# Performance work log

Measured on AMD Instinct MI355X. Metric: run time of the kernel, lower is better.

The kernel has to match this reference:

```python
import jax, jax.numpy as jnp
import numpy as np

B, NX, NY = 4, 128, 128
DIM, DH, HEADS, LATENT, DOUT = 128, 64, 8, 64, 128
KM = 3
KD = DH * KM          # per-head low-rank-kernel dim (192)
SCALING = 1.0         # kernel_multiplier<=4 and softmax=False -> scaling_factor
ROT_SCALE = 64.0      # 1/min_freq of continuous RotaryEmbedding (min_freq=1/64)
EPS = 1e-5


def layer_norm(x, g, b):
    m = x.mean(-1, keepdims=True)
    v = jnp.var(x, axis=-1, keepdims=True)
    return (x - m) * jax.lax.rsqrt(v + EPS) * g + b


def pooling_reducer(x, Win, g, b, W1, b1, W2, b2):
    # x: [b, n, m, c] -> mean over axis 2 -> PreNorm(MLP with gated GELU) -> [b, n, latent]
    h = (x @ Win).mean(axis=2)
    h = layer_norm(h, g, b)
    h = h @ W1 + b1
    c = h.shape[-1] // 2
    h = jax.nn.gelu(h[..., :c], approximate=False) * h[..., c:]
    return h @ W2 + b2


def rotary(t, pos):
    # t: [b,h,n,d], pos: [n] continuous coordinates
    d = t.shape[-1]
    inv_freq = 1.0 / (10000.0 ** (jnp.arange(0, d, 2, dtype=jnp.float32) / d))
    f = (pos * ROT_SCALE)[:, None] * inv_freq          # [n, d//2]
    f = jnp.concatenate([f, f], axis=-1)               # [n, d]
    cos, sin = jnp.cos(f), jnp.sin(f)
    x1, x2 = jnp.split(t, 2, axis=-1)
    rot = jnp.concatenate([-x2, x1], axis=-1)          # rotate_half (half-split variant)
    return t * cos + rot * sin


def low_rank_kernel(u, pos, Wqk):
    # u: [b, n, latent] -> kernel K: [b, h, n, n]
    b, n, _ = u.shape
    qk = u @ Wqk                                       # [b, n, 2*h*KD]
    q, k = jnp.split(qk, 2, axis=-1)
    q = q.reshape(b, n, HEADS, KD).transpose(0, 2, 1, 3)
    k = k.reshape(b, n, HEADS, KD).transpose(0, 2, 1, 3)
    q = rotary(q, pos)
    k = rotary(k, pos)
    return jnp.einsum('bhid,bhjd->bhij', q, k) * SCALING


def setup_inputs():
    key = jax.random.key(0)
    ks = jax.random.split(key, 16)
    s = 0.02
    def rn(k, shape):
        return jax.random.normal(k, shape, dtype=jnp.float32) * s
    return {
        'u': jax.random.normal(ks[0], (B, NX, NY, DIM), dtype=jnp.float32),
        'pos_x': jnp.sort(jax.random.uniform(ks[1], (NX,), dtype=jnp.float32)),
        'pos_y': jnp.sort(jax.random.uniform(ks[2], (NY,), dtype=jnp.float32)),
        'ln_g': jnp.ones((DIM,), jnp.float32),
        'ln_b': jnp.zeros((DIM,), jnp.float32),
        'Wv': rn(ks[3], (DIM, HEADS * DH)),
        'Win': rn(ks[4], (DIM, DIM)),
        'px_Win': rn(ks[5], (DIM, DIM)),
        'px_g': jnp.ones((DIM,), jnp.float32),
        'px_b': jnp.zeros((DIM,), jnp.float32),
        'px_W1': rn(ks[6], (DIM, 2 * DIM)),
        'px_b1': jnp.zeros((2 * DIM,), jnp.float32),
        'px_W2': rn(ks[7], (DIM, LATENT)),
        'px_b2': jnp.zeros((LATENT,), jnp.float32),
        'py_Win': rn(ks[8], (DIM, DIM)),
        'py_g': jnp.ones((DIM,), jnp.float32),
        'py_b': jnp.zeros((DIM,), jnp.float32),
        'py_W1': rn(ks[9], (DIM, 2 * DIM)),
        'py_b1': jnp.zeros((2 * DIM,), jnp.float32),
        'py_W2': rn(ks[10], (DIM, LATENT)),
        'py_b2': jnp.zeros((LATENT,), jnp.float32),
        'Wqk_x': rn(ks[11], (LATENT, 2 * HEADS * KD)),
        'Wqk_y': rn(ks[12], (LATENT, 2 * HEADS * KD)),
        'Wo1': rn(ks[13], (HEADS * DH, DOUT)),
        'Wo2': rn(ks[14], (DOUT, DOUT)),
    }


def reference(u, pos_x, pos_y, ln_g, ln_b, Wv, Win,
              px_Win, px_g, px_b, px_W1, px_b1, px_W2, px_b2,
              py_Win, py_g, py_b, py_W1, py_b1, py_W2, py_b2,
              Wqk_x, Wqk_y, Wo1, Wo2):
    un = layer_norm(u, ln_g, ln_b)                      # [b,nx,ny,dim]
    v = un @ Wv                                         # [b,nx,ny,h*dh]
    ui = un @ Win
    ux = pooling_reducer(ui, px_Win, px_g, px_b, px_W1, px_b1, px_W2, px_b2)                       # [b,nx,L]
    uy = pooling_reducer(ui.transpose(0, 2, 1, 3), py_Win, py_g, py_b, py_W1, py_b1, py_W2, py_b2)  # [b,ny,L]
    kx = low_rank_kernel(ux, pos_x, Wqk_x)              # [b,h,nx,nx]
    ky = low_rank_kernel(uy, pos_y, Wqk_y)              # [b,h,ny,ny]
    b, nx, ny, _ = u.shape
    vphi = v.reshape(b, nx, ny, HEADS, DH).transpose(0, 3, 1, 2, 4)   # b h i l c
    t = jnp.einsum('bhij,bhjmc->bhimc', kx, vphi)       # attend along x axis
    t = jnp.einsum('bhlm,bhimc->bhilc', ky, t)          # attend along y axis
    t = t.transpose(0, 2, 3, 1, 4).reshape(b, nx, ny, HEADS * DH)
    # InstanceNorm2d applied to a channels-LAST tensor (as in the original repo):
    # torch treats dim1 (nx) as channels, normalizing over (ny, h*dh) per (b, nx), no affine.
    m = t.mean(axis=(2, 3), keepdims=True)
    var = t.var(axis=(2, 3), keepdims=True)
    t = (t - m) * jax.lax.rsqrt(var + EPS)
    h = jax.nn.gelu(t @ Wo1, approximate=False)
    return h @ Wo2
```

## Files before the change

kernel.cpp:

```cpp
#include <hip/hip_runtime.h>
#include <math.h>

#define KDD 192

typedef __attribute__((ext_vector_type(8))) short bfrag;
typedef __attribute__((ext_vector_type(4))) float facc;

__device__ inline unsigned short bf16r(float x) {
  union { float f; unsigned u; } v; v.f = x;
  unsigned r = v.u + 0x7fffu + ((v.u >> 16) & 1u);
  return (unsigned short)(r >> 16);
}
__device__ inline float bf2f(unsigned short h) {
  union { unsigned u; float f; } v; v.u = ((unsigned)h) << 16; return v.f;
}
__device__ inline float gelu_f(float x) {
  return x * 0.5f * (1.f + erff(x * 0.70710678f));
}
__device__ __forceinline__ void gload16(const void* g, void* l) {
  __builtin_amdgcn_global_load_lds((const __attribute__((address_space(1))) unsigned int*)g,
                                   (__attribute__((address_space(3))) unsigned int*)l,
                                   16, 0, 0);
}

__global__ __launch_bounds__(256) void k_lnw(const float* __restrict__ x,
                                             const float* __restrict__ g,
                                             const float* __restrict__ bb,
                                             unsigned short* __restrict__ y,
                                             const float* __restrict__ Wv,
                                             const float* __restrict__ Wo1,
                                             const float* __restrict__ Wo2,
                                             unsigned short* __restrict__ WvT,
                                             unsigned short* __restrict__ Wo1T,
                                             unsigned short* __restrict__ Wo2T,
                                             float* __restrict__ scol,
                                             const float* __restrict__ Win,
                                             const float* __restrict__ pxW,
                                             const float* __restrict__ pyW,
                                             float* __restrict__ Wcx,
                                             float* __restrict__ Wcy,
                                             const float* __restrict__ pos_x,
                                             const float* __restrict__ pos_y,
                                             float* __restrict__ tabx,
                                             float* __restrict__ taby) {
  __shared__ float As[16][64];
  __shared__ float Bs[16][64];
  int bid = blockIdx.x, t = threadIdx.x;
  if (bid < 16384) {
    int w = t >> 6, lane = t & 63;
    size_t row = (size_t)bid * 4 + w;
    float2 v = *(const float2*)(x + row * 128 + lane * 2);
    float s = v.x + v.y, s2 = v.x * v.x + v.y * v.y;
#pragma unroll
    for (int off = 1; off < 64; off <<= 1) {
      s += __shfl_xor(s, off, 64);
      s2 += __shfl_xor(s2, off, 64);
    }
    float mean = s * (1.f / 128.f);
    float var = s2 * (1.f / 128.f) - mean * mean;
    float r = rsqrtf(var + 1e-5f);
    float2 gg = *(const float2*)(g + lane * 2);
    float2 bv = *(const float2*)(bb + lane * 2);
    unsigned h0 = bf16r((v.x - mean) * r * gg.x + bv.x);
    unsigned h1 = bf16r((v.y - mean) * r * gg.y + bv.y);
    *(unsigned*)(y + row * 128 + lane * 2) = h0 | (h1 << 16);
    return;
  }
  if (bid < 16961) {
    int blk = bid - 16384;
    if (blk < 256) {
      int idx = blk * 256 + t;
      int c = idx >> 7, r = idx & 127;
      WvT[(size_t)c * 128 + r] = bf16r(Wv[(size_t)r * 512 + c]);
    } else if (blk < 512) {
      int idx = (blk - 256) * 256 + t;
      int n = idx >> 9, k = idx & 511;
      Wo1T[(size_t)n * 512 + k] = bf16r(Wo1[(size_t)k * 128 + n]);
    } else if (blk < 576) {
      int idx = (blk - 512) * 256 + t;
      int n = idx >> 7, k = idx & 127;
      Wo2T[n * 128 + k] = bf16r(Wo2[k * 128 + n]);
    } else {
      if (t < 128) {
        float a = 0;
        for (int k = 0; k < 512; k++) a += bf2f(bf16r(Wo1[k * 128 + t]));
        scol[t] = a;
      }
    }
    return;
  }
  if (bid < 16969) {
    int idx = bid - 16961;
    int n0 = (idx & 1) * 64, m0 = ((idx >> 1) & 1) * 64;
    const float* A = Win;
    const float* Bm = (idx >> 2) ? pyW : pxW;
    float* C = (idx >> 2) ? Wcy : Wcx;
    int tx = t & 15, ty = t >> 4;
    float acc[4][4] = {};
    int la_m = t >> 2, la_k = (t & 3) * 4;
    int lb_k = t >> 4, lb_n = (t & 15) * 4;
    for (int k0 = 0; k0 < 128; k0 += 16) {
      float4 a4 = *(const float4*)(A + (size_t)(m0 + la_m) * 128 + k0 + la_k);
      As[la_k + 0][la_m] = a4.x; As[la_k + 1][la_m] = a4.y;
      As[la_k + 2][la_m] = a4.z; As[la_k + 3][la_m] = a4.w;
      float4 b4 = *(const float4*)(Bm + (size_t)(k0 + lb_k) * 128 + n0 + lb_n);
      *(float4*)&Bs[lb_k][lb_n] = b4;
      __syncthreads();
#pragma unroll
      for (int kk = 0; kk < 16; kk++) {
        float4 av = *(const float4*)&As[kk][ty * 4];
        float4 bv = *(const float4*)&Bs[kk][tx * 4];
        float a[4] = {av.x, av.y, av.z, av.w};
        float b[4] = {bv.x, bv.y, bv.z, bv.w};
#pragma unroll
        for (int i = 0; i < 4; i++)
#pragma unroll
          for (int j = 0; j < 4; j++) acc[i][j] += a[i] * b[j];
      }
      __syncthreads();
    }
#pragma unroll
    for (int i = 0; i < 4; i++) {
      float4 o;
      o.x = acc[i][0]; o.y = acc[i][1]; o.z = acc[i][2]; o.w = acc[i][3];
      *(float4*)(C + (size_t)(m0 + ty * 4 + i) * 128 + n0 + tx * 4) = o;
    }
    return;
  }
  {
    int id = (bid - 16969) * 256 + t;
    int axis = id >= 12288;
    int rem = axis ? id - 12288 : id;
    int n = rem / 96, fi = rem - n * 96;
    const float* pos = axis ? pos_y : pos_x;
    float inv = expf(-logf(10000.f) * ((float)fi / 96.f));
    float f = pos[n] * 64.f * inv;
    float2 cssn;
    cssn.x = cosf(f);
    cssn.y = sinf(f);
    ((float2*)(axis ? taby : tabx))[n * 96 + fi] = cssn;
  }
}

__global__ __launch_bounds__(128) void k_pool2(const unsigned short* __restrict__ un,
                                               const float* __restrict__ Wc0, const float* __restrict__ Wc1,
                                               const float* __restrict__ g0, const float* __restrict__ g1,
                                               const float* __restrict__ bb0, const float* __restrict__ bb1,
                                               const float* __restrict__ W10, const float* __restrict__ W11,
                                               const float* __restrict__ b10, const float* __restrict__ b11,
                                               const float* __restrict__ W20, const float* __restrict__ W21,
                                               const float* __restrict__ b20, const float* __restrict__ b21,
                                               float* __restrict__ o0, float* __restrict__ o1) {
  int sel = blockIdx.y;
  const float* Wc = sel ? Wc1 : Wc0;
  const float* g = sel ? g1 : g0;     const float* bb = sel ? bb1 : bb0;
  const float* W1 = sel ? W11 : W10;  const float* b1 = sel ? b11 : b10;
  const float* W2 = sel ? W21 : W20;  const float* b2 = sel ? b21 : b20;
  float* out = sel ? o1 : o0;
  int row = blockIdx.x;
  int t = threadIdx.x;
  __shared__ float xin[128], h1[128], h3[128];
  __shared__ float ps[2], ps2[2];
  {
    float s0 = 0.f;
    if (sel == 0) {
      const unsigned short* p = un + (size_t)row * 16384 + t;
      for (int j = 0; j < 128; j++) s0 += bf2f(p[(size_t)j * 128]);
    } else {
      int b = row >> 7, j = row & 127;
      const unsigned short* p = un + (size_t)b * 2097152 + (size_t)j * 128 + t;
      for (int i = 0; i < 128; i++) s0 += bf2f(p[(size_t)i * 16384]);
    }
    xin[t] = s0 * (1.f / 128.f);
  }
  __syncthreads();
  float a = 0;
  for (int k = 0; k < 128; k++) a += xin[k] * Wc[k * 128 + t];
  float s = a, s2 = a * a;
  for (int off = 32; off > 0; off >>= 1) {
    s += __shfl_down(s, off, 64);
    s2 += __shfl_down(s2, off, 64);
  }
  if ((t & 63) == 0) { ps[t >> 6] = s; ps2[t >> 6] = s2; }
  __syncthreads();
  float S = ps[0] + ps[1], S2 = ps2[0] + ps2[1];
  float mean = S * (1.f / 128.f);
  float var = S2 * (1.f / 128.f) - mean * mean;
  float r = rsqrtf(var + 1e-5f);
  h1[t] = (a - mean) * r * g[t] + bb[t];
  __syncthreads();
  float u1 = b1[t], u2 = b1[t + 128];
  for (int k = 0; k < 128; k++) {
    float hv = h1[k];
    u1 += hv * W1[k * 256 + t];
    u2 += hv * W1[k * 256 + t + 128];
  }
  h3[t] = gelu_f(u1) * u2;
  __syncthreads();
  if (t < 64) {
    float o = b2[t];
    for (int k = 0; k < 128; k++) o += h3[k] * W2[k * 64 + t];
    out[(size_t)row * 64 + t] = o;
  }
}

__global__ __launch_bounds__(256) void k_gemmz(const float* __restrict__ A0,
                                               const float* __restrict__ B0,
                                               float* __restrict__ C0,
                                               const float* __restrict__ A1,
                                               const float* __restrict__ B1,
                                               float* __restrict__ C1,
                                               int K, int lda, int ldb, int ldc) {
  const float* A = blockIdx.z ? A1 : A0;
  const float* Bm = blockIdx.z ? B1 : B0;
  float* C = blockIdx.z ? C1 : C0;
  __shared__ float As[16][64];
  __shared__ float Bs[16][64];
  int tid = threadIdx.x;
  int n0 = blockIdx.x * 64, m0 = blockIdx.y * 64;
  int tx = tid & 15, ty = tid >> 4;
  float acc[4][4] = {};
  int la_m = tid >> 2, la_k = (tid & 3) * 4;
  int lb_k = tid >> 4, lb_n = (tid & 15) * 4;
  for (int k0 = 0; k0 < K; k0 += 16) {
    float4 a4 = *(const float4*)(A + (size_t)(m0 + la_m) * lda + k0 + la_k);
    As[la_k + 0][la_m] = a4.x; As[la_k + 1][la_m] = a4.y;
    As[la_k + 2][la_m] = a4.z; As[la_k + 3][la_m] = a4.w;
    float4 b4 = *(const float4*)(Bm + (size_t)(k0 + lb_k) * ldb + n0 + lb_n);
    *(float4*)&Bs[lb_k][lb_n] = b4;
    __syncthreads();
#pragma unroll
    for (int kk = 0; kk < 16; kk++) {
      float4 av = *(const float4*)&As[kk][ty * 4];
      float4 bv = *(const float4*)&Bs[kk][tx * 4];
      float a[4] = {av.x, av.y, av.z, av.w};
      float b[4] = {bv.x, bv.y, bv.z, bv.w};
#pragma unroll
      for (int i = 0; i < 4; i++)
#pragma unroll
        for (int j = 0; j < 4; j++) acc[i][j] += a[i] * b[j];
    }
    __syncthreads();
  }
#pragma unroll
  for (int i = 0; i < 4; i++) {
    float4 o;
    o.x = acc[i][0]; o.y = acc[i][1]; o.z = acc[i][2]; o.w = acc[i][3];
    *(float4*)(C + (size_t)(m0 + ty * 4 + i) * ldc + n0 + tx * 4) = o;
  }
}

__global__ __launch_bounds__(512) void k_qkt2(const float* __restrict__ qk0, const float* __restrict__ qk1,
                                              const float* __restrict__ tab0, const float* __restrict__ tab1,
                                              unsigned short* __restrict__ C0,
                                              unsigned short* __restrict__ C1) {
  int z = blockIdx.z;
  int bh = z & 31;
  int b = bh >> 3, h = bh & 7;
  const float* qk = (z < 32) ? qk0 : qk1;
  const float* tab = (z < 32) ? tab0 : tab1;
  unsigned short* Cb = ((z < 32) ? C0 : C1) + (size_t)bh * 16384;
  __shared__ float As[16][64];
  __shared__ float Bs[16][64];
  int tid = threadIdx.x;
  int i0 = blockIdx.y * 64, j0 = blockIdx.x * 64;
  int tx = tid & 15, ty = tid >> 4;
  float acc[2][4] = {};
  int l_m = tid >> 3, l_k = (tid & 7) * 2;
  for (int k0 = 0; k0 < KDD; k0 += 16) {
    int d = k0 + l_k;
    int fi = d < 96 ? d : d - 96;
    float sgn = d < 96 ? -1.f : 1.f;
    int prt = d < 96 ? d + 96 : d - 96;
    {
      int n = i0 + l_m;
      const float* src = qk + (size_t)(b * 128 + n) * 3072 + h * 192;
      float2 qd = *(const float2*)(src + d);
      float2 qp = *(const float2*)(src + prt);
      float2 t0 = *(const float2*)(tab + (size_t)(n * 96 + fi) * 2);
      float2 t1 = *(const float2*)(tab + (size_t)(n * 96 + fi + 1) * 2);
      As[l_k + 0][l_m] = qd.x * t0.x + sgn * qp.x * t0.y;
      As[l_k + 1][l_m] = qd.y * t1.x + sgn * qp.y * t1.y;
    }
    {
      int n = j0 + l_m;
      const float* src = qk + (size_t)(b * 128 + n) * 3072 + 1536 + h * 192;
      float2 qd = *(const float2*)(src + d);
      float2 qp = *(const float2*)(src + prt);
      float2 t0 = *(const float2*)(tab + (size_t)(n * 96 + fi) * 2);
      float2 t1 = *(const float2*)(tab + (size_t)(n * 96 + fi + 1) * 2);
      Bs[l_k + 0][l_m] = qd.x * t0.x + sgn * qp.x * t0.y;
      Bs[l_k + 1][l_m] = qd.y * t1.x + sgn * qp.y * t1.y;
    }
    __syncthreads();
#pragma unroll
    for (int kk = 0; kk < 16; kk++) {
      float2 av = *(const float2*)&As[kk][ty * 2];
      float4 bv = *(const float4*)&Bs[kk][tx * 4];
      float a[2] = {av.x, av.y};
      float b2[4] = {bv.x, bv.y, bv.z, bv.w};
#pragma unroll
      for (int i = 0; i < 2; i++)
#pragma unroll
        for (int j = 0; j < 4; j++) acc[i][j] += a[i] * b2[j];
    }
    __syncthreads();
  }
#pragma unroll
  for (int i = 0; i < 2; i++) {
    unsigned h0 = bf16r(acc[i][0]), h1 = bf16r(acc[i][1]);
    unsigned h2 = bf16r(acc[i][2]), h3 = bf16r(acc[i][3]);
    uint2 pk;
    pk.x = h0 | (h1 << 16);
    pk.y = h2 | (h3 << 16);
    *(uint2*)(Cb + (size_t)(i0 + ty * 2 + i) * 128 + j0 + tx * 4) = pk;
  }
}


__global__ __launch_bounds__(256) void k_vt(const unsigned short* __restrict__ WvT,
                                            const unsigned short* __restrict__ un,
                                            unsigned short* __restrict__ vT) {
  int nt = blockIdx.x;
  __shared__ __align__(16) unsigned short Bs[16384];
  int tid = threadIdx.x;
  int w = tid >> 6, lane = tid & 63, quad = lane >> 4, l16 = lane & 15;
  int wr = w >> 1, wc = w & 1;
  {
    const unsigned short* sbp = un + (size_t)nt * 16384;
#pragma unroll
    for (int q = 0; q < 8; q++) {
      int rbase = w * 32 + q * 4;
      int r = rbase + quad;
      gload16(sbp + (size_t)r * 128 + ((l16 ^ (r & 15)) << 3), &Bs[rbase * 128]);
    }
  }
  __syncthreads();
  facc zf = {0.f, 0.f, 0.f, 0.f};
#pragma unroll
  for (int mt = 0; mt < 4; mt++) {
    const unsigned short* ap = WvT + (size_t)mt * 128 * 128;
    facc acc[4][4];
#pragma unroll
    for (int lt = 0; lt < 4; lt++)
#pragma unroll
      for (int xt = 0; xt < 4; xt++) acc[lt][xt] = zf;
#pragma unroll
    for (int k0 = 0; k0 < 4; k0++) {
      int chunk = ((k0 * 4 + quad) ^ l16) << 3;
      bfrag bv[4], av[4];
#pragma unroll
      for (int lt = 0; lt < 4; lt++)
        bv[lt] = *(const bfrag*)&Bs[((wc * 4 + lt) * 16 + l16) * 128 + chunk];
#pragma unroll
      for (int xt = 0; xt < 4; xt++)
        av[xt] = *(const bfrag*)(ap + (size_t)((wr * 4 + xt) * 16 + l16) * 128 + k0 * 32 + quad * 8);
      __builtin_amdgcn_s_setprio(1);
#pragma unroll
      for (int lt = 0; lt < 4; lt++)
#pragma unroll
        for (int xt = 0; xt < 4; xt++)
          acc[lt][xt] = __builtin_amdgcn_mfma_f32_16x16x32_bf16(bv[lt], av[xt], acc[lt][xt], 0, 0, 0);
      __builtin_amdgcn_s_setprio(0);
    }
#pragma unroll
    for (int xt = 0; xt < 4; xt++) {
      int hc = mt * 128 + (wr * 4 + xt) * 16 + l16;
      unsigned short* dst = vT + (size_t)hc * 65536 + nt * 128 + quad * 4;
#pragma unroll
      for (int lt = 0; lt < 4; lt++) {
        facc a = acc[lt][xt];
        uint2 p;
        p.x = (unsigned)bf16r(a[0]) | ((unsigned)bf16r(a[1]) << 16);
        p.y = (unsigned)bf16r(a[2]) | ((unsigned)bf16r(a[3]) << 16);
        *(uint2*)(dst + (wc * 4 + lt) * 16) = p;
      }
    }
  }
}

__global__ __launch_bounds__(256, 2) void k_fuse12(const unsigned short* __restrict__ kxall,
                                                   const unsigned short* __restrict__ kyall,
                                                   const unsigned short* __restrict__ vT,
                                                   unsigned short* __restrict__ ttp,
                                                   float* __restrict__ sb,
                                                   float* __restrict__ s2b) {
  int blk = blockIdx.x;
  int bh = blk >> 4, strip = blk & 15;
  int b = bh >> 3, h = bh & 7;
  __shared__ __align__(16) unsigned short Ky[16384];
  __shared__ __align__(16) unsigned short Vs[16384];
  int tid = threadIdx.x;
  int w = tid >> 6, lane = tid & 63, quad = lane >> 4, l16 = lane & 15;
  int wr = w >> 1, wc = w & 1;

  {
    const unsigned short* kb = kyall + (size_t)bh * 16384;
#pragma unroll
    for (int q = 0; q < 8; q++) {
      int rbase = w * 32 + q * 4;
      int r = rbase + quad;
      gload16(kb + (size_t)r * 128 + ((l16 ^ (r & 15)) << 3), &Ky[rbase * 128]);
    }
  }
  bfrag axf[4][4];
  {
    const unsigned short* xb = kxall + (size_t)bh * 16384;
#pragma unroll
    for (int it = 0; it < 4; it++) {
      int i = (wr * 4 + it) * 16 + l16;
#pragma unroll
      for (int k0 = 0; k0 < 4; k0++)
        axf[it][k0] = *(const bfrag*)(xb + (size_t)i * 128 + k0 * 32 + quad * 8);
    }
  }

  float s[4] = {0.f, 0.f, 0.f, 0.f}, s2[4] = {0.f, 0.f, 0.f, 0.f};
  facc zf = {0.f, 0.f, 0.f, 0.f};

  for (int cc = 0; cc < 4; cc++) {
    int c = strip * 4 + cc;
    if (cc) __syncthreads();
    {
      const unsigned short* vb = vT + (size_t)(h * 64 + c) * 65536 + (size_t)b * 16384;
#pragma unroll
      for (int q = 0; q < 8; q++) {
        int rbase = w * 32 + q * 4;
        int r = rbase + quad;
        gload16(vb + (size_t)r * 128 + ((l16 ^ (r & 15)) << 3), &Vs[rbase * 128]);
      }
    }
    __syncthreads();

    facc a1[4][4];
#pragma unroll
    for (int xt = 0; xt < 4; xt++)
#pragma unroll
      for (int lt = 0; lt < 4; lt++) a1[xt][lt] = zf;
#pragma unroll
    for (int k0 = 0; k0 < 4; k0++) {
      int chunk = ((k0 * 4 + quad) ^ l16) << 3;
      bfrag av[4], bv[4];
#pragma unroll
      for (int xt = 0; xt < 4; xt++)
        av[xt] = *(const bfrag*)&Vs[((wr * 4 + xt) * 16 + l16) * 128 + chunk];
#pragma unroll
      for (int lt = 0; lt < 4; lt++)
        bv[lt] = *(const bfrag*)&Ky[((wc * 4 + lt) * 16 + l16) * 128 + chunk];
      __builtin_amdgcn_s_setprio(1);
#pragma unroll
      for (int xt = 0; xt < 4; xt++)
#pragma unroll
        for (int lt = 0; lt < 4; lt++)
          a1[xt][lt] = __builtin_amdgcn_mfma_f32_16x16x32_bf16(av[xt], bv[lt], a1[xt][lt], 0, 0, 0);
      __builtin_amdgcn_s_setprio(0);
    }
    __syncthreads();
#pragma unroll
    for (int xt = 0; xt < 4; xt++) {
      int xc = (wr * 4 + xt) * 2 + (quad >> 1);
      int xo = (quad & 1) * 4;
#pragma unroll
      for (int lt = 0; lt < 4; lt++) {
        int l = (wc * 4 + lt) * 16 + l16;
        unsigned p0 = (unsigned)bf16r(a1[xt][lt][0]) | ((unsigned)bf16r(a1[xt][lt][1]) << 16);
        unsigned p1 = (unsigned)bf16r(a1[xt][lt][2]) | ((unsigned)bf16r(a1[xt][lt][3]) << 16);
        uint2 p; p.x = p0; p.y = p1;
        *(uint2*)&Vs[l * 128 + ((xc ^ (l & 15)) << 3) + xo] = p;
      }
    }
    __syncthreads();

    facc a2[4][4];
#pragma unroll
    for (int st = 0; st < 4; st++)
#pragma unroll
      for (int it = 0; it < 4; it++) a2[st][it] = zf;
#pragma unroll
    for (int k0 = 0; k0 < 4; k0++) {
      int chunk = ((k0 * 4 + quad) ^ l16) << 3;
      bfrag sv[4];
#pragma unroll
      for (int st = 0; st < 4; st++)
        sv[st] = *(const bfrag*)&Vs[((wc * 4 + st) * 16 + l16) * 128 + chunk];
      __builtin_amdgcn_s_setprio(1);
#pragma unroll
      for (int st = 0; st < 4; st++)
#pragma unroll
        for (int it = 0; it < 4; it++)
          a2[st][it] = __builtin_amdgcn_mfma_f32_16x16x32_bf16(sv[st], axf[it][k0], a2[st][it], 0, 0, 0);
      __builtin_amdgcn_s_setprio(0);
    }
    {
      unsigned short* dst = ttp + ((size_t)(bh * 64 + c) << 14);
#pragma unroll
      for (int st = 0; st < 4; st++) {
        int l0 = (wc * 4 + st) * 16 + quad * 4;
#pragma unroll
        for (int it = 0; it < 4; it++) {
          int i = (wr * 4 + it) * 16 + l16;
          float f0 = a2[st][it][0], f1 = a2[st][it][1];
          float f2 = a2[st][it][2], f3 = a2[st][it][3];
          unsigned p0 = (unsigned)bf16r(f0) | ((unsigned)bf16r(f1) << 16);
          unsigned p1 = (unsigned)bf16r(f2) | ((unsigned)bf16r(f3) << 16);
          uint2 p; p.x = p0; p.y = p1;
          *(uint2*)(dst + (size_t)i * 128 + l0) = p;
          s[it] += (f0 + f1) + (f2 + f3);
          s2[it] += f0 * f0 + f1 * f1 + f2 * f2 + f3 * f3;
        }
      }
    }
  }
#pragma unroll
  for (int it = 0; it < 4; it++) {
    float v = s[it], v2 = s2[it];
    v += __shfl_xor(v, 16, 64);  v += __shfl_xor(v, 32, 64);
    v2 += __shfl_xor(v2, 16, 64); v2 += __shfl_xor(v2, 32, 64);
    if (quad == 0) {
      int i = (wr * 4 + it) * 16 + l16;
      atomicAdd(&sb[b * 128 + i], v);
      atomicAdd(&s2b[b * 128 + i], v2);
    }
  }
}

__global__ __launch_bounds__(256) void k_tail2(const unsigned short* __restrict__ ttp,
                                               const unsigned short* __restrict__ Wo1T,
                                               const unsigned short* __restrict__ Wo2T,
                                               float* __restrict__ out,
                                               const float* __restrict__ sb,
                                               const float* __restrict__ s2b,
                                               const float* __restrict__ sc) {
  int blk = blockIdx.x;
  int b = blk >> 7, i = blk & 127;
  __shared__ __align__(16) unsigned short As[16384];
  __shared__ __align__(16) unsigned short Bs[16384];
  int tid = threadIdx.x;
  int w = tid >> 6, lane = tid & 63, quad = lane >> 4, l16 = lane & 15;
  facc zf = {0.f, 0.f, 0.f, 0.f};
  facc a1[2][8];
#pragma unroll
  for (int a = 0; a < 2; a++)
#pragma unroll
    for (int bq = 0; bq < 8; bq++) a1[a][bq] = zf;
  for (int kc = 0; kc < 4; kc++) {
    if (kc) __syncthreads();
    {
      int r = tid >> 1, half = tid & 1;
      int hc = kc * 128 + r;
      const unsigned short* src = ttp + (((size_t)(b * 8 + (hc >> 6)) * 64 + (hc & 63)) * 128 + i) * 128 + half * 64;
#pragma unroll
      for (int q = 0; q < 8; q++) {
        uint4 v = *(const uint4*)(src + q * 8);
        unsigned short* pv = (unsigned short*)&v;
#pragma unroll
        for (int e = 0; e < 8; e++) {
          int l = half * 64 + q * 8 + e;
          As[l * 128 + (((r >> 3) ^ (l & 15)) << 3) + (r & 7)] = pv[e];
        }
      }
      const unsigned short* sB = Wo1T + (size_t)r * 512 + kc * 128 + half * 64;
#pragma unroll
      for (int q = 0; q < 8; q++) {
        int c8 = half * 8 + q;
        *(uint4*)&Bs[r * 128 + ((c8 ^ (r & 15)) << 3)] = *(const uint4*)(sB + q * 8);
      }
    }
    __syncthreads();
#pragma unroll
    for (int k0 = 0; k0 < 4; k0++) {
      bfrag av[2];
#pragma unroll
      for (int it = 0; it < 2; it++) {
        int row = (w + it * 4) * 16 + l16;
        av[it] = *(const bfrag*)&As[row * 128 + (((k0 * 4 + quad) ^ l16) << 3)];
      }
#pragma unroll
      for (int nt = 0; nt < 8; nt++) {
        int row = nt * 16 + l16;
        bfrag bv = *(const bfrag*)&Bs[row * 128 + (((k0 * 4 + quad) ^ l16) << 3)];
        a1[0][nt] = __builtin_amdgcn_mfma_f32_16x16x32_bf16(av[0], bv, a1[0][nt], 0, 0, 0);
        a1[1][nt] = __builtin_amdgcn_mfma_f32_16x16x32_bf16(av[1], bv, a1[1][nt], 0, 0, 0);
      }
    }
  }
  float S = sb[b * 128 + i], S2 = s2b[b * 128 + i];
  float mean = S * (1.f / 65536.f);
  float var = S2 * (1.f / 65536.f) - mean * mean;
  float rs = rsqrtf(var + 1e-5f);
  __syncthreads();
#pragma unroll
  for (int it = 0; it < 2; it++)
#pragma unroll
    for (int nt = 0; nt < 8; nt++) {
      int n1 = nt * 16 + l16;
      float scn = sc[n1];
#pragma unroll
      for (int rr = 0; rr < 4; rr++) {
        int l = (w + it * 4) * 16 + quad * 4 + rr;
        float val = (a1[it][nt][rr] - mean * scn) * rs;
        As[l * 128 + (((n1 >> 3) ^ (l & 15)) << 3) + (n1 & 7)] = bf16r(gelu_f(val));
      }
    }
  {
    int r = tid >> 1, half = tid & 1;
    const unsigned short* sB = Wo2T + (size_t)r * 128 + half * 64;
#pragma unroll
    for (int q = 0; q < 8; q++) {
      int c8 = half * 8 + q;
      *(uint4*)&Bs[r * 128 + ((c8 ^ (r & 15)) << 3)] = *(const uint4*)(sB + q * 8);
    }
  }
  __syncthreads();
  facc a2[2][8];
#pragma unroll
  for (int a = 0; a < 2; a++)
#pragma unroll
    for (int bq = 0; bq < 8; bq++) a2[a][bq] = zf;
#pragma unroll
  for (int k0 = 0; k0 < 4; k0++) {
    bfrag av[2];
#pragma unroll
    for (int it = 0; it < 2; it++) {
      int row = (w + it * 4) * 16 + l16;
      av[it] = *(const bfrag*)&As[row * 128 + (((k0 * 4 + quad) ^ l16) << 3)];
    }
#pragma unroll
    for (int nt = 0; nt < 8; nt++) {
      int row = nt * 16 + l16;
      bfrag bv = *(const bfrag*)&Bs[row * 128 + (((k0 * 4 + quad) ^ l16) << 3)];
      a2[0][nt] = __builtin_amdgcn_mfma_f32_16x16x32_bf16(av[0], bv, a2[0][nt], 0, 0, 0);
      a2[1][nt] = __builtin_amdgcn_mfma_f32_16x16x32_bf16(av[1], bv, a2[1][nt], 0, 0, 0);
    }
  }
#pragma unroll
  for (int it = 0; it < 2; it++)
#pragma unroll
    for (int nt = 0; nt < 8; nt++) {
      int n2 = nt * 16 + l16;
#pragma unroll
      for (int rr = 0; rr < 4; rr++) {
        int l = (w + it * 4) * 16 + quad * 4 + rr;
        out[((size_t)(b * 16384 + i * 128 + l)) * 128 + n2] = a2[it][nt][rr];
      }
    }
}

extern "C" void kernel_launch(void* const* d_in, const int* in_sizes, int n_in,
                              void* d_out, int out_size, void* d_ws, size_t ws_size,
                              hipStream_t stream) {
  const float* u = (const float*)d_in[0];
  const float* pos_x = (const float*)d_in[1];
  const float* pos_y = (const float*)d_in[2];
  const float* ln_g = (const float*)d_in[3];
  const float* ln_b = (const float*)d_in[4];
  const float* Wv = (const float*)d_in[5];
  const float* Win = (const float*)d_in[6];
  const float* px_Win = (const float*)d_in[7];
  const float* px_g = (const float*)d_in[8];
  const float* px_b = (const float*)d_in[9];
  const float* px_W1 = (const float*)d_in[10];
  const float* px_b1 = (const float*)d_in[11];
  const float* px_W2 = (const float*)d_in[12];
  const float* px_b2 = (const float*)d_in[13];
  const float* py_Win = (const float*)d_in[14];
  const float* py_g = (const float*)d_in[15];
  const float* py_b = (const float*)d_in[16];
  const float* py_W1 = (const float*)d_in[17];
  const float* py_b1 = (const float*)d_in[18];
  const float* py_W2 = (const float*)d_in[19];
  const float* py_b2 = (const float*)d_in[20];
  const float* Wqk_x = (const float*)d_in[21];
  const float* Wqk_y = (const float*)d_in[22];
  const float* Wo1 = (const float*)d_in[23];
  const float* Wo2 = (const float*)d_in[24];
  float* out = (float*)d_out;

  const size_t NEED = 44868736;
  if (ws_size < NEED * sizeof(float)) return;
  float* ws = (float*)d_ws;
  unsigned short* un_bf = (unsigned short*)ws;
  unsigned short* vT    = (unsigned short*)(ws + 4194304);
  unsigned short* ttp   = (unsigned short*)(ws + 20971520);
  float* small = ws + 37748736;
  float* Wcx   = small + 131072;
  float* Wcy   = small + 147456;
  float* ux    = small + 163840;
  float* uy    = small + 196608;
  float* qkx   = small + 229376;
  float* qky   = small + 1802240;
  float* tabx  = small + 3375104;
  float* taby  = small + 3399680;
  unsigned short* kx_bf = (unsigned short*)(small + 6520832);
  unsigned short* ky_bf = (unsigned short*)(small + 6782976);
  unsigned short* WvT   = (unsigned short*)(small + 7045120);
  unsigned short* Wo1T  = (unsigned short*)(small + 7077888);
  unsigned short* Wo2T  = (unsigned short*)(small + 7110656);
  float* sbuf  = small + 7118848;
  float* s2buf = small + 7119360;
  float* scol  = small + 7119872;

  hipMemsetAsync(sbuf, 0, 1024 * sizeof(float), stream);

  k_lnw<<<17065, 256, 0, stream>>>(u, ln_g, ln_b, un_bf, Wv, Wo1, Wo2,
                                   WvT, Wo1T, Wo2T, scol,
                                   Win, px_Win, py_Win, Wcx, Wcy,
                                   pos_x, pos_y, tabx, taby);
  k_pool2<<<dim3(512, 2), 128, 0, stream>>>(un_bf, Wcx, Wcy, px_g, py_g, px_b, py_b,
                                            px_W1, py_W1, px_b1, py_b1, px_W2, py_W2,
                                            px_b2, py_b2, ux, uy);
  k_gemmz<<<dim3(48, 8, 2), 256, 0, stream>>>(ux, Wqk_x, qkx, uy, Wqk_y, qky,
                                              64, 64, 3072, 3072);
  k_qkt2<<<dim3(2, 2, 64), 512, 0, stream>>>(qkx, qky, tabx, taby, kx_bf, ky_bf);

  k_vt<<<512, 256, 0, stream>>>(WvT, un_bf, vT);
  k_fuse12<<<512, 256, 0, stream>>>(kx_bf, ky_bf, vT, ttp, sbuf, s2buf);
  k_tail2<<<512, 256, 0, stream>>>(ttp, Wo1T, Wo2T, out, sbuf, s2buf, scol);
}
```

Before: 296.3 us.

## Merge pooling into V-projection kernel, fold memset into LN, pack tail transpose stores

Drops the separate memset by having an extra block of the LN kernel zero the statistics buffer. The pooling-reducer kernel and the V-projection GEMM now share one launch, with each pooling block handling two rows, which removes a kernel and lets the two independent stages run at once. The tail kernel's transposed LDS staging now writes two rows per 32-bit store instead of single 16-bit stores. The cost is a larger shared-memory footprint for the pooling blocks, which carry the GEMM's LDS allocation.

```diff
diff --git a/kernel.cpp b/kernel.cpp
--- a/kernel.cpp
+++ b/kernel.cpp
@@ -42,7 +42,8 @@
                                              const float* __restrict__ pos_x,
                                              const float* __restrict__ pos_y,
                                              float* __restrict__ tabx,
-                                             float* __restrict__ taby) {
+                                             float* __restrict__ taby,
+                                             float* __restrict__ sbuf) {
   __shared__ float As[16][64];
   __shared__ float Bs[16][64];
   int bid = blockIdx.x, t = threadIdx.x;
@@ -127,7 +128,7 @@
     }
     return;
   }
-  {
+  if (bid < 17065) {
     int id = (bid - 16969) * 256 + t;
     int axis = id >= 12288;
     int rem = axis ? id - 12288 : id;
@@ -139,28 +140,96 @@
     cssn.x = cosf(f);
     cssn.y = sinf(f);
     ((float2*)(axis ? taby : tabx))[n * 96 + fi] = cssn;
-  }
-}
-
-__global__ __launch_bounds__(128) void k_pool2(const unsigned short* __restrict__ un,
-                                               const float* __restrict__ Wc0, const float* __restrict__ Wc1,
-                                               const float* __restrict__ g0, const float* __restrict__ g1,
-                                               const float* __restrict__ bb0, const float* __restrict__ bb1,
-                                               const float* __restrict__ W10, const float* __restrict__ W11,
-                                               const float* __restrict__ b10, const float* __restrict__ b11,
-                                               const float* __restrict__ W20, const float* __restrict__ W21,
-                                               const float* __restrict__ b20, const float* __restrict__ b21,
-                                               float* __restrict__ o0, float* __restrict__ o1) {
-  int sel = blockIdx.y;
+    return;
+  }
+  {
+    float4 z4 = {0.f, 0.f, 0.f, 0.f};
+    ((float4*)sbuf)[t] = z4;
+  }
+}
+
+__global__ __launch_bounds__(256) void k_pvt(const unsigned short* __restrict__ WvT,
+                                             const unsigned short* __restrict__ un,
+                                             unsigned short* __restrict__ vT,
+                                             const float* __restrict__ Wc0, const float* __restrict__ Wc1,
+                                             const float* __restrict__ g0, const float* __restrict__ g1,
+                                             const float* __restrict__ bb0, const float* __restrict__ bb1,
+                                             const float* __restrict__ W10, const float* __restrict__ W11,
+                                             const float* __restrict__ b10, const float* __restrict__ b11,
+                                             const float* __restrict__ W20, const float* __restrict__ W21,
+                                             const float* __restrict__ b20, const float* __restrict__ b21,
+                                             float* __restrict__ o0, float* __restrict__ o1) {
+  __shared__ __align__(16) unsigned short Bs[16384];
+  __shared__ float xin[2][128], h1[2][128], h3[2][128];
+  __shared__ float ps[2][2], ps2[2][2];
+  int bid = blockIdx.x;
+  int tid = threadIdx.x;
+  if (bid < 512) {
+    int nt = bid;
+    int w = tid >> 6, lane = tid & 63, quad = lane >> 4, l16 = lane & 15;
+    int wr = w >> 1, wc = w & 1;
+    {
+      const unsigned short* sbp = un + (size_t)nt * 16384;
+#pragma unroll
+      for (int q = 0; q < 8; q++) {
+        int rbase = w * 32 + q * 4;
+        int r = rbase + quad;
+        gload16(sbp + (size_t)r * 128 + ((l16 ^ (r & 15)) << 3), &Bs[rbase * 128]);
+      }
+    }
+    __syncthreads();
+    facc zf = {0.f, 0.f, 0.f, 0.f};
+#pragma unroll
+    for (int mt = 0; mt < 4; mt++) {
+      const unsigned short* ap = WvT + (size_t)mt * 128 * 128;
+      facc acc[4][4];
+#pragma unroll
+      for (int lt = 0; lt < 4; lt++)
+#pragma unroll
+        for (int xt = 0; xt < 4; xt++) acc[lt][xt] = zf;
+#pragma unroll
+      for (int k0 = 0; k0 < 4; k0++) {
+        int chunk = ((k0 * 4 + quad) ^ l16) << 3;
+        bfrag bv[4], av[4];
+#pragma unroll
+        for (int lt = 0; lt < 4; lt++)
+          bv[lt] = *(const bfrag*)&Bs[((wc * 4 + lt) * 16 + l16) * 128 + chunk];
+#pragma unroll
+        for (int xt = 0; xt < 4; xt++)
+          av[xt] = *(const bfrag*)(ap + (size_t)((wr * 4 + xt) * 16 + l16) * 128 + k0 * 32 + quad * 8);
+        __builtin_amdgcn_s_setprio(1);
+#pragma unroll
+        for (int lt = 0; lt < 4; lt++)
+#pragma unroll
+          for (int xt = 0; xt < 4; xt++)
+            acc[lt][xt] = __builtin_amdgcn_mfma_f32_16x16x32_bf16(bv[lt], av[xt], acc[lt][xt], 0, 0, 0);
+        __builtin_amdgcn_s_setprio(0);
+      }
+#pragma unroll
+      for (int xt = 0; xt < 4; xt++) {
+        int hc = mt * 128 + (wr * 4 + xt) * 16 + l16;
+        unsigned short* dst = vT + (size_t)hc * 65536 + nt * 128 + quad * 4;
+#pragma unroll
+        for (int lt = 0; lt < 4; lt++) {
+          facc a = acc[lt][xt];
+          uint2 p;
+          p.x = (unsigned)bf16r(a[0]) | ((unsigned)bf16r(a[1]) << 16);
+          p.y = (unsigned)bf16r(a[2]) | ((unsigned)bf16r(a[3]) << 16);
+          *(uint2*)(dst + (wc * 4 + lt) * 16) = p;
+        }
+      }
+    }
+    return;
+  }
+  int u2 = tid >> 7;
+  int t = tid & 127;
+  int unit = (bid - 512) * 2 + u2;
+  int sel = unit >> 9, row = unit & 511;
   const float* Wc = sel ? Wc1 : Wc0;
   const float* g = sel ? g1 : g0;     const float* bb = sel ? bb1 : bb0;
   const float* W1 = sel ? W11 : W10;  const float* b1 = sel ? b11 : b10;
   const float* W2 = sel ? W21 : W20;  const float* b2 = sel ? b21 : b20;
   float* out = sel ? o1 : o0;
-  int row = blockIdx.x;
-  int t = threadIdx.x;
-  __shared__ float xin[128], h1[128], h3[128];
-  __shared__ float ps[2], ps2[2];
   {
     float s0 = 0.f;
     if (sel == 0) {
@@ -171,35 +240,35 @@
       const unsigned short* p = un + (size_t)b * 2097152 + (size_t)j * 128 + t;
       for (int i = 0; i < 128; i++) s0 += bf2f(p[(size_t)i * 16384]);
     }
-    xin[t] = s0 * (1.f / 128.f);
+    xin[u2][t] = s0 * (1.f / 128.f);
   }
   __syncthreads();
   float a = 0;
-  for (int k = 0; k < 128; k++) a += xin[k] * Wc[k * 128 + t];
+  for (int k = 0; k < 128; k++) a += xin[u2][k] * Wc[k * 128 + t];
   float s = a, s2 = a * a;
   for (int off = 32; off > 0; off >>= 1) {
     s += __shfl_down(s, off, 64);
     s2 += __shfl_down(s2, off, 64);
   }
-  if ((t & 63) == 0) { ps[t >> 6] = s; ps2[t >> 6] = s2; }
+  if ((t & 63) == 0) { ps[u2][t >> 6] = s; ps2[u2][t >> 6] = s2; }
   __syncthreads();
-  float S = ps[0] + ps[1], S2 = ps2[0] + ps2[1];
+  float S = ps[u2][0] + ps[u2][1], S2 = ps2[u2][0] + ps2[u2][1];
   float mean = S * (1.f / 128.f);
   float var = S2 * (1.f / 128.f) - mean * mean;
   float r = rsqrtf(var + 1e-5f);
-  h1[t] = (a - mean) * r * g[t] + bb[t];
+  h1[u2][t] = (a - mean) * r * g[t] + bb[t];
   __syncthreads();
-  float u1 = b1[t], u2 = b1[t + 128];
+  float u1 = b1[t], uu2 = b1[t + 128];
   for (int k = 0; k < 128; k++) {
-    float hv = h1[k];
+    float hv = h1[u2][k];
     u1 += hv * W1[k * 256 + t];
-    u2 += hv * W1[k * 256 + t + 128];
-  }
-  h3[t] = gelu_f(u1) * u2;
+    uu2 += hv * W1[k * 256 + t + 128];
+  }
+  h3[u2][t] = gelu_f(u1) * uu2;
   __syncthreads();
   if (t < 64) {
     float o = b2[t];
-    for (int k = 0; k < 128; k++) o += h3[k] * W2[k * 64 + t];
+    for (int k = 0; k < 128; k++) o += h3[u2][k] * W2[k * 64 + t];
     out[(size_t)row * 64 + t] = o;
   }
 }
@@ -318,67 +387,6 @@
 }
 
 
-__global__ __launch_bounds__(256) void k_vt(const unsigned short* __restrict__ WvT,
-                                            const unsigned short* __restrict__ un,
-                                            unsigned short* __restrict__ vT) {
-  int nt = blockIdx.x;
-  __shared__ __align__(16) unsigned short Bs[16384];
-  int tid = threadIdx.x;
-  int w = tid >> 6, lane = tid & 63, quad = lane >> 4, l16 = lane & 15;
-  int wr = w >> 1, wc = w & 1;
-  {
-    const unsigned short* sbp = un + (size_t)nt * 16384;
-#pragma unroll
-    for (int q = 0; q < 8; q++) {
-      int rbase = w * 32 + q * 4;
-      int r = rbase + quad;
-      gload16(sbp + (size_t)r * 128 + ((l16 ^ (r & 15)) << 3), &Bs[rbase * 128]);
-    }
-  }
-  __syncthreads();
-  facc zf = {0.f, 0.f, 0.f, 0.f};
-#pragma unroll
-  for (int mt = 0; mt < 4; mt++) {
-    const unsigned short* ap = WvT + (size_t)mt * 128 * 128;
-    facc acc[4][4];
-#pragma unroll
-    for (int lt = 0; lt < 4; lt++)
-#pragma unroll
-      for (int xt = 0; xt < 4; xt++) acc[lt][xt] = zf;
-#pragma unroll
-    for (int k0 = 0; k0 < 4; k0++) {
-      int chunk = ((k0 * 4 + quad) ^ l16) << 3;
-      bfrag bv[4], av[4];
-#pragma unroll
-      for (int lt = 0; lt < 4; lt++)
-        bv[lt] = *(const bfrag*)&Bs[((wc * 4 + lt) * 16 + l16) * 128 + chunk];
-#pragma unroll
-      for (int xt = 0; xt < 4; xt++)
-        av[xt] = *(const bfrag*)(ap + (size_t)((wr * 4 + xt) * 16 + l16) * 128 + k0 * 32 + quad * 8);
-      __builtin_amdgcn_s_setprio(1);
-#pragma unroll
-      for (int lt = 0; lt < 4; lt++)
-#pragma unroll
-        for (int xt = 0; xt < 4; xt++)
-          acc[lt][xt] = __builtin_amdgcn_mfma_f32_16x16x32_bf16(bv[lt], av[xt], acc[lt][xt], 0, 0, 0);
-      __builtin_amdgcn_s_setprio(0);
-    }
-#pragma unroll
-    for (int xt = 0; xt < 4; xt++) {
-      int hc = mt * 128 + (wr * 4 + xt) * 16 + l16;
-      unsigned short* dst = vT + (size_t)hc * 65536 + nt * 128 + quad * 4;
-#pragma unroll
-      for (int lt = 0; lt < 4; lt++) {
-        facc a = acc[lt][xt];
-        uint2 p;
-        p.x = (unsigned)bf16r(a[0]) | ((unsigned)bf16r(a[1]) << 16);
-        p.y = (unsigned)bf16r(a[2]) | ((unsigned)bf16r(a[3]) << 16);
-        *(uint2*)(dst + (wc * 4 + lt) * 16) = p;
-      }
-    }
-  }
-}
-
 __global__ __launch_bounds__(256, 2) void k_fuse12(const unsigned short* __restrict__ kxall,
                                                    const unsigned short* __restrict__ kyall,
                                                    const unsigned short* __restrict__ vT,
@@ -546,19 +554,27 @@
   for (int kc = 0; kc < 4; kc++) {
     if (kc) __syncthreads();
     {
+      int rp = tid >> 2, qh = tid & 3;
+      int r0 = rp * 2, r1 = r0 + 1;
+      int hc0 = kc * 128 + r0, hc1 = kc * 128 + r1;
+      const unsigned short* s0 = ttp + (((size_t)(b * 8 + (hc0 >> 6)) * 64 + (hc0 & 63)) * 128 + i) * 128 + qh * 32;
+      const unsigned short* s1 = ttp + (((size_t)(b * 8 + (hc1 >> 6)) * 64 + (hc1 & 63)) * 128 + i) * 128 + qh * 32;
+      int swz = ((r0 >> 3) << 3) + (r0 & 7);
+#pragma unroll
+      for (int q = 0; q < 4; q++) {
+        uint4 v0 = *(const uint4*)(s0 + q * 8);
+        uint4 v1 = *(const uint4*)(s1 + q * 8);
+        unsigned short* p0 = (unsigned short*)&v0;
+        unsigned short* p1 = (unsigned short*)&v1;
+#pragma unroll
+        for (int e = 0; e < 8; e++) {
+          int l = qh * 32 + q * 8 + e;
+          int idx = l * 128 + ((((r0 >> 3) ^ (l & 15)) << 3)) + (r0 & 7);
+          *(unsigned*)&As[idx] = (unsigned)p0[e] | ((unsigned)p1[e] << 16);
+        }
+      }
+      (void)swz;
       int r = tid >> 1, half = tid & 1;
-      int hc = kc * 128 + r;
-      const unsigned short* src = ttp + (((size_t)(b * 8 + (hc >> 6)) * 64 + (hc & 63)) * 128 + i) * 128 + half * 64;
-#pragma unroll
-      for (int q = 0; q < 8; q++) {
-        uint4 v = *(const uint4*)(src + q * 8);
-        unsigned short* pv = (unsigned short*)&v;
-#pragma unroll
-        for (int e = 0; e < 8; e++) {
-          int l = half * 64 + q * 8 + e;
-          As[l * 128 + (((r >> 3) ^ (l & 15)) << 3) + (r & 7)] = pv[e];
-        }
-      }
       const unsigned short* sB = Wo1T + (size_t)r * 512 + kc * 128 + half * 64;
 #pragma unroll
       for (int q = 0; q < 8; q++) {
@@ -700,20 +716,18 @@
   float* s2buf = small + 7119360;
   float* scol  = small + 7119872;
 
-  hipMemsetAsync(sbuf, 0, 1024 * sizeof(float), stream);
-
-  k_lnw<<<17065, 256, 0, stream>>>(u, ln_g, ln_b, un_bf, Wv, Wo1, Wo2,
+  k_lnw<<<17066, 256, 0, stream>>>(u, ln_g, ln_b, un_bf, Wv, Wo1, Wo2,
                                    WvT, Wo1T, Wo2T, scol,
                                    Win, px_Win, py_Win, Wcx, Wcy,
-                                   pos_x, pos_y, tabx, taby);
-  k_pool2<<<dim3(512, 2), 128, 0, stream>>>(un_bf, Wcx, Wcy, px_g, py_g, px_b, py_b,
-                                            px_W1, py_W1, px_b1, py_b1, px_W2, py_W2,
-                                            px_b2, py_b2, ux, uy);
+                                   pos_x, pos_y, tabx, taby, sbuf);
+  k_pvt<<<1024, 256, 0, stream>>>(WvT, un_bf, vT,
+                                  Wcx, Wcy, px_g, py_g, px_b, py_b,
+                                  px_W1, py_W1, px_b1, py_b1, px_W2, py_W2,
+                                  px_b2, py_b2, ux, uy);
   k_gemmz<<<dim3(48, 8, 2), 256, 0, stream>>>(ux, Wqk_x, qkx, uy, Wqk_y, qky,
                                               64, 64, 3072, 3072);
   k_qkt2<<<dim3(2, 2, 64), 512, 0, stream>>>(qkx, qky, tabx, taby, kx_bf, ky_bf);
 
-  k_vt<<<512, 256, 0, stream>>>(WvT, un_bf, vT);
   k_fuse12<<<512, 256, 0, stream>>>(kx_bf, ky_bf, vT, ttp, sbuf, s2buf);
   k_tail2<<<512, 256, 0, stream>>>(ttp, Wo1T, Wo2T, out, sbuf, s2buf, scol);
 }
```

Result: faster. 286.7 us (-3.2%).
